# Kernel tuning notes

Hardware: AMD Instinct MI355X
Metric: run time of the kernel (lower is better)

## Reference

```python
import jax, jax.numpy as jnp
import numpy as np

SR = 22050
L = 65537            # signal length; chosen so rfft length == L (required by source broadcast)
NFFT = 131072        # 2**ceil(log2(L))
RLEN = NFFT // 2 + 1 # == L
OUT_SIZE = 65537     # output_size init arg
BANDS = [("delta", 1.0, 4.0), ("theta", 4.0, 8.0), ("alpha", 8.0, 13.0),
         ("beta", 13.0, 30.0), ("gamma", 30.0, 100.0), ("high_gamma", 100.0, 200.0)]
SPEC = [("schumann", 7.83), ("healing", 528.0), ("solfeggio", 396.0), ("sleep", 2.5),
        ("focus", 14.1), ("harmony", 432.0), ("meditation", 6.0), ("energy", 30.0)]
FREQS_NP = np.fft.rfftfreq(NFFT, d=1.0 / SR).astype(np.float32)


def _prog_mean(hp, W1, b1, W2, b2, W3, b3):
    # vectorized get_harmonic_progression(arange(L)).mean()
    t = jnp.arange(L, dtype=jnp.float32)
    tn = (t / OUT_SIZE)[:, None]                       # [L,1]
    h = jax.nn.relu(tn @ W1 + b1)
    h = jax.nn.relu(h @ W2 + b2)
    mp = h @ W3 + b3                                   # [L,8]
    mod_depth = mp[0, 1]
    chord_idx = jnp.floor(t * 8.0 / OUT_SIZE).astype(jnp.int32) % 8
    chord = hp[chord_idx]                              # [L,4]
    chord = chord * (1.0 + mod_depth * jnp.sin(2.0 * jnp.pi * t / OUT_SIZE))[:, None]
    return chord.mean()


def _gain(bw, fw, hp, W1, b1, W2, b2, W3, b3):
    # all modulation is data-independent -> single [RLEN] multiplicative gain
    t = jnp.arange(L, dtype=jnp.float32)
    gain = jnp.ones(RLEN, dtype=jnp.float32)
    for k, (_, low, high) in enumerate(BANDS):
        center = (low + high) / 2.0
        width = (high - low) / 2.0
        m_np = np.exp(-0.5 * ((FREQS_NP - center) / (width / 2.0)) ** 2)
        m_np[(FREQS_NP < low) | (FREQS_NP > high)] = 0.0
        if not np.any(m_np > 0.01):  # static branch (mask is data-independent)
            continue
        mask = jnp.asarray(m_np.astype(np.float32))     # [RLEN] == [L]
        time_mod = jnp.sin(2.0 * jnp.pi * center * t / SR)
        gain = gain * (1.0 + mask * bw[k] * (1.0 + 0.2 * time_mod))
    pm = _prog_mean(hp, W1, b1, W2, b2, W3, b3)
    ws = min(15, NFFT // 100)
    ws = ws if ws > 0 else 1
    for j, (_, f) in enumerate(SPEC):
        if f >= SR / 2:
            continue
        for mult in (1.0, 2.0, 3.0, 4.0, 5.0):
            hf = f * mult
            if hf >= SR / 2:
                continue
            hidx = int(np.argmin(np.abs(FREQS_NP - hf)))
            s = max(0, hidx - ws)
            e = min(RLEN - 1, hidx + ws)
            if s >= e:
                continue
            idxs = np.arange(s, e + 1)
            win = jnp.asarray(np.exp(-0.5 * ((idxs - hidx) / (ws / 3.0)) ** 2).astype(np.float32))
            enh = fw[j] * win * (1.0 / mult ** 1.2) * (1.0 + pm)
            gain = gain.at[s:e + 1].multiply(1.0 + enh)
    return gain


def _forward(x, bw, fw, hp, W1, b1, W2, b2, W3, b3):
    gain = _gain(bw, fw, hp, W1, b1, W2, b2, W3, b3)    # [RLEN]
    xp = jnp.pad(x, ((0, 0), (0, 0), (0, NFFT - L)))    # zero-pad to n_fft
    X = jnp.fft.rfft(xp, axis=-1) * gain                # [B,C,RLEN] complex
    mag = jnp.abs(X)
    ph = jnp.angle(X)
    mid = 0.7 * mag[..., 1:-1] + 0.15 * mag[..., :-2] + 0.15 * mag[..., 2:]
    mag_s = jnp.concatenate([mag[..., :1], mid, mag[..., -1:]], axis=-1)
    Xc = mag_s * jnp.exp(1j * ph)
    y = jnp.fft.irfft(Xc, n=NFFT, axis=-1)[..., :L]
    return y.astype(x.dtype)


def setup_inputs() -> dict:
    key = jax.random.key(0)
    ks = jax.random.split(key, 8)
    B, C = 128, 2
    x = jax.random.normal(ks[0], (B, C, L), dtype=jnp.float32)
    band_weights = jnp.full((6,), 0.5, dtype=jnp.float32)
    freq_weights = jnp.full((8,), 0.3, dtype=jnp.float32)
    harmonic_progression = jax.random.normal(ks[1], (8, 4), dtype=jnp.float32)
    W1 = jax.random.normal(ks[2], (1, 32), dtype=jnp.float32)
    b1 = jnp.zeros((32,), dtype=jnp.float32)
    W2 = jax.random.normal(ks[3], (32, 16), dtype=jnp.float32) * (1.0 / np.sqrt(32.0))
    b2 = jnp.zeros((16,), dtype=jnp.float32)
    W3 = jax.random.normal(ks[4], (16, 8), dtype=jnp.float32) * (1.0 / np.sqrt(16.0))
    b3 = jnp.zeros((8,), dtype=jnp.float32)
    return {"x": x, "band_weights": band_weights, "freq_weights": freq_weights,
            "harmonic_progression": harmonic_progression,
            "W1": W1, "b1": b1, "W2": W2, "b2": b2, "W3": W3, "b3": b3}


def reference(x, band_weights, freq_weights, harmonic_progression, W1, b1, W2, b2, W3, b3):
    return _forward(x, band_weights, freq_weights, harmonic_progression, W1, b1, W2, b2, W3, b3)
```

## Files before the change

### kernel.cpp

```cpp
#include <hip/hip_runtime.h>
#include <hip/hip_fp16.h>
#include <math.h>

#define L_SIG 65537
#define NH    65536
#define NSIG  256
#define PI_F  3.14159265358979323846f

struct alignas(8) c32 { float x, y; };
typedef __half2 h2;
__device__ __forceinline__ c32 mkc(float a, float b){ c32 r; r.x=a; r.y=b; return r; }
__device__ __forceinline__ c32 cadd(c32 a, c32 b){ return mkc(a.x+b.x, a.y+b.y); }
__device__ __forceinline__ c32 csub(c32 a, c32 b){ return mkc(a.x-b.x, a.y-b.y); }
__device__ __forceinline__ c32 cmul(c32 a, c32 b){ return mkc(a.x*b.x - a.y*b.y, a.x*b.y + a.y*b.x); }
__device__ __forceinline__ h2  c2h(c32 a){ return __floats2half2_rn(a.x, a.y); }
__device__ __forceinline__ c32 h2c(h2 a){ float2 f = __half22float2(a); return mkc(f.x, f.y); }

template<int S>
__device__ __forceinline__ void fft16(c32 v[16]) {
  constexpr float C16[16] = {
    1.0f, 0.9238795325112867f, 0.7071067811865476f, 0.3826834323650898f,
    0.0f,-0.3826834323650898f,-0.7071067811865476f,-0.9238795325112867f,
   -1.0f,-0.9238795325112867f,-0.7071067811865476f,-0.3826834323650898f,
    0.0f, 0.3826834323650898f, 0.7071067811865476f, 0.9238795325112867f };
  constexpr float S16[16] = {
    0.0f, 0.3826834323650898f, 0.7071067811865476f, 0.9238795325112867f,
    1.0f, 0.9238795325112867f, 0.7071067811865476f, 0.3826834323650898f,
    0.0f,-0.3826834323650898f,-0.7071067811865476f,-0.9238795325112867f,
   -1.0f,-0.9238795325112867f,-0.7071067811865476f,-0.3826834323650898f };
  c32 s[16];
  #pragma unroll
  for (int b0 = 0; b0 < 4; ++b0) {
    c32 x0=v[b0], x1=v[b0+4], x2=v[b0+8], x3=v[b0+12];
    c32 u0=cadd(x0,x2), u1=csub(x0,x2), u2=cadd(x1,x3), u3=csub(x1,x3);
    c32 iu3 = mkc(-u3.y, u3.x);
    c32 yy[4];
    yy[0]=cadd(u0,u2); yy[2]=csub(u0,u2);
    if (S < 0) { yy[1]=csub(u1,iu3); yy[3]=cadd(u1,iu3); }
    else       { yy[1]=cadd(u1,iu3); yy[3]=csub(u1,iu3); }
    #pragma unroll
    for (int c0 = 0; c0 < 4; ++c0) {
      const int p = (b0*c0) & 15;
      c32 w = mkc(C16[p], (S<0) ? -S16[p] : S16[p]);
      s[c0*4 + b0] = cmul(yy[c0], w);
    }
  }
  #pragma unroll
  for (int c0 = 0; c0 < 4; ++c0) {
    c32 x0=s[c0*4+0], x1=s[c0*4+1], x2=s[c0*4+2], x3=s[c0*4+3];
    c32 u0=cadd(x0,x2), u1=csub(x0,x2), u2=cadd(x1,x3), u3=csub(x1,x3);
    c32 iu3 = mkc(-u3.y, u3.x);
    c32 yy[4];
    yy[0]=cadd(u0,u2); yy[2]=csub(u0,u2);
    if (S < 0) { yy[1]=csub(u1,iu3); yy[3]=cadd(u1,iu3); }
    else       { yy[1]=cadd(u1,iu3); yy[3]=csub(u1,iu3); }
    v[c0+0]=yy[0]; v[c0+4]=yy[1]; v[c0+8]=yy[2]; v[c0+12]=yy[3];
  }
}

template<int S>
__device__ __forceinline__ void fft256_team(c32 v[16], int r, int t, c32* sc) {
  fft16<S>(v);
  float ang = (float)S * (2.0f*PI_F/256.0f) * (float)r;
  c32 st; __sincosf(ang, &st.y, &st.x);
  c32 w = st;
  #pragma unroll
  for (int c = 1; c < 16; ++c) { v[c] = cmul(v[c], w); w = cmul(w, st); }
  __syncthreads();
  #pragma unroll
  for (int c = 0; c < 16; ++c) {
    int idx = c*256 + ((r*16 + t) ^ ((c & 3) << 3));
    sc[idx] = v[c];
  }
  __syncthreads();
  #pragma unroll
  for (int a = 0; a < 16; ++a) {
    int idx = r*256 + ((a*16 + t) ^ ((r & 3) << 3));
    v[a] = sc[idx];
  }
  fft16<S>(v);
}

__global__ __launch_bounds__(256) void k_pm(const float* __restrict__ hp,
                                            float* __restrict__ pm_part) {
  __shared__ float r0[256], r1[256];
  int t = threadIdx.x, b = blockIdx.x;
  int gid = b*256 + t;
  float s0 = 0.f, s1 = 0.f;
  for (int tt = gid; tt < 65537; tt += 16384) {
    int ci = (tt * 8) / 65537;
    float cs = hp[ci*4+0] + hp[ci*4+1] + hp[ci*4+2] + hp[ci*4+3];
    float ang = (6.2831853071795864769f * (float)tt) / 65537.0f;
    s0 += cs;
    s1 += cs * sinf(ang);
  }
  r0[t] = s0; r1[t] = s1;
  __syncthreads();
  for (int s = 128; s > 0; s >>= 1) {
    if (t < s) { r0[t] += r0[t+s]; r1[t] += r1[t+s]; }
    __syncthreads();
  }
  if (t == 0) { pm_part[2*b] = r0[0]; pm_part[2*b+1] = r1[0]; }
}

__global__ __launch_bounds__(256) void k_prep2(const float* __restrict__ b1,
    const float* __restrict__ W2, const float* __restrict__ b2,
    const float* __restrict__ W3, const float* __restrict__ b3,
    const float* __restrict__ fw, const float* __restrict__ pm_part,
    float* __restrict__ pm_out, int* __restrict__ hidx, float* __restrict__ amp) {
  __shared__ float r0[64], r1[64];
  __shared__ float s_pm;
  int t = threadIdx.x;
  if (t < 64) { r0[t] = pm_part[2*t]; r1[t] = pm_part[2*t+1]; }
  __syncthreads();
  if (t == 0) {
    float h1[32], h2v[16];
    for (int i=0;i<32;i++){ float z = b1[i]; h1[i] = z > 0.f ? z : 0.f; }
    for (int o=0;o<16;o++){ float acc = b2[o];
      for (int i=0;i<32;i++) acc += h1[i]*W2[i*16+o];
      h2v[o] = acc > 0.f ? acc : 0.f; }
    float md = b3[1];
    for (int i=0;i<16;i++) md += h2v[i]*W3[i*8+1];
    float S0 = 0.f, S1 = 0.f;
    for (int i=0;i<64;i++){ S0 += r0[i]; S1 += r1[i]; }
    s_pm = (S0 + md*S1) / (65537.0f * 4.0f);
    pm_out[0] = s_pm;
  }
  __syncthreads();
  if (t < 40) {
    const double SPECF[8] = {7.83, 528.0, 396.0, 2.5, 14.1, 432.0, 6.0, 30.0};
    int j = t / 5, mi = t % 5;
    double mult = (double)(mi + 1);
    double hf = SPECF[j] * mult;
    double ratio = hf * (131072.0 / 22050.0);
    hidx[t] = (int)floor(ratio + 0.5);
    amp[t] = (float)((double)fw[j] * pow(mult, -1.2) * (1.0 + (double)s_pm));
  }
}

__global__ __launch_bounds__(256) void k_gain(float* __restrict__ gain,
    const float* __restrict__ bw, const int* __restrict__ hidx,
    const float* __restrict__ amp) {
  int i = blockIdx.x*256 + threadIdx.x;
  if (i >= 65537) return;
  float f = (float)((double)i * (22050.0/131072.0));
  float g = 1.0f;
  constexpr double LO[6] = {1,4,8,13,30,100};
  constexpr double HI[6] = {4,8,13,30,100,200};
  #pragma unroll
  for (int k = 0; k < 6; ++k) {
    float center = (float)(0.5*(LO[k]+HI[k]));
    float sig    = (float)(0.25*(HI[k]-LO[k]));
    float dm = (f - center)/sig;
    float mask = expf(-0.5f*dm*dm);
    if (f < (float)LO[k] || f > (float)HI[k]) mask = 0.f;
    float ang = (float)(6.283185307179586*0.5*(LO[k]+HI[k])) * (float)i / 22050.0f;
    g *= 1.0f + mask * bw[k] * (1.0f + 0.2f*sinf(ang));
  }
  for (int l = 0; l < 40; ++l) {
    int d = i - hidx[l];
    if (d >= -15 && d <= 15) {
      float dd = (float)d * 0.2f;
      g *= 1.0f + amp[l] * expf(-0.5f*dd*dd);
    }
  }
  gain[i] = g;
}

__global__ __launch_bounds__(256) void k_fwd1(const float* __restrict__ x,
                                              h2* __restrict__ A, int s0) {
  __shared__ c32 sc[4096];
  int b = blockIdx.x; int sl = b >> 4; int g = b & 15;
  int t = threadIdx.x & 15, r = threadIdx.x >> 4;
  int n1 = g*16 + t;
  const float* xb = x + (size_t)(s0 + sl) * L_SIG;
  c32 v[16];
  #pragma unroll
  for (int j = 0; j < 16; ++j) {
    int n = n1 + 256*r + 4096*j;
    c32 z = mkc(0.f, 0.f);
    if (n < 32768)       { z.x = xb[2*n]; z.y = xb[2*n+1]; }
    else if (n == 32768) { z.x = xb[65536]; }
    v[j] = z;
  }
  fft256_team<-1>(v, r, t, sc);
  float a0 = -(2.0f*PI_F/65536.0f) * (float)(n1 * r);
  float a1 = -(2.0f*PI_F/4096.0f)  * (float)n1;
  c32 wb, wst;
  __sincosf(a0, &wb.y, &wb.x);
  __sincosf(a1, &wst.y, &wst.x);
  #pragma unroll
  for (int j = 0; j < 16; ++j) { v[j] = cmul(v[j], wb); wb = cmul(wb, wst); }
  __syncthreads();
  #pragma unroll
  for (int j = 0; j < 16; ++j)
    sc[(r + 16*j)*16 + t] = v[j];
  __syncthreads();
  h2* Ab = A + (size_t)sl * NH;
  int u = threadIdx.x & 15, k2b = threadIdx.x >> 4;
  #pragma unroll
  for (int m = 0; m < 16; ++m) {
    int k2 = k2b + 16*m;
    Ab[(size_t)k2*256 + g*16 + u] = c2h(sc[k2*16 + u]);
  }
}

__global__ __launch_bounds__(256) void k_fwd2(const h2* __restrict__ A,
                                              h2* __restrict__ B) {
  __shared__ c32 sc[4096];
  h2* stg = (h2*)sc;
  int b = blockIdx.x; int sl = b >> 4; int g = b & 15;
  int tid = threadIdx.x;
  int t = tid & 15, r = tid >> 4;
  const h2* Ab = A + (size_t)sl * NH;
  #pragma unroll
  for (int m = 0; m < 4; ++m) {
    int flat = tid + 256*m;
    int row = flat >> 6, i = flat & 63;
    float4 z = ((const float4*)(Ab + (size_t)(g*16 + row)*256))[i];
    *((float4*)&stg[row*260 + 4*i]) = z;
  }
  __syncthreads();
  c32 v[16];
  #pragma unroll
  for (int j = 0; j < 16; ++j)
    v[j] = h2c(stg[t*260 + r + 16*j]);
  fft256_team<-1>(v, r, t, sc);
  h2* Bb = B + (size_t)sl * NH;
  int k2 = g*16 + t;
  #pragma unroll
  for (int j = 0; j < 16; ++j) Bb[(size_t)k2 + 256*(r + 16*j)] = c2h(v[j]);
}

__global__ __launch_bounds__(256) void k_mid(const h2* __restrict__ Z,
    h2* __restrict__ Zc, const float* __restrict__ gain) {
  __shared__ c32 XL[258], XH[258];
  __shared__ float ML[258], MH[258];
  __shared__ float TC[258], TS[258];
  int b = blockIdx.x; int s = b >> 7; int blk = b & 127;
  int k0 = blk << 8;
  const h2* Zs = Z + (size_t)s * NH;
  h2* Os = Zc + (size_t)s * NH;
  int t = threadIdx.x;
  for (int e = t; e < 258; e += 256) {
    int k = k0 - 1 + e;
    bool kv = (k >= 0);
    int kc = kv ? k : 0;
    c32 zk = h2c(Zs[k & (NH-1)]);
    c32 zb = h2c(Zs[(NH - k) & (NH-1)]);
    c32 Aa = mkc(0.5f*(zk.x + zb.x), 0.5f*(zk.y - zb.y));
    c32 Bm = mkc(0.5f*(zk.x - zb.x), 0.5f*(zk.y + zb.y));
    float sn, cn; __sincosf((PI_F/65536.0f)*(float)k, &sn, &cn);
    TC[e] = cn; TS[e] = sn;
    c32 wB = cmul(mkc(-sn, -cn), Bm);
    float gk = gain[kc];
    float gK = gain[NH - kc];
    c32 Xk = mkc((Aa.x + wB.x)*gk,  (Aa.y + wB.y)*gk);
    c32 XK = mkc((Aa.x - wB.x)*gK, -(Aa.y - wB.y)*gK);
    float nk = Xk.x*Xk.x + Xk.y*Xk.y;
    float nK = XK.x*XK.x + XK.y*XK.y;
    float rk = rsqrtf(nk), rK = rsqrtf(nK);
    c32 Uk = (nk > 0.f) ? mkc(Xk.x*rk, Xk.y*rk) : mkc(1.f, 0.f);
    c32 UK = (nK > 0.f) ? mkc(XK.x*rK, XK.y*rK) : mkc(1.f, 0.f);
    float mk = (kv && nk > 0.f) ? nk*rk : 0.f;
    float mK = (kv && nK > 0.f) ? nK*rK : 0.f;
    XL[e] = Uk;  ML[e] = mk;
    XH[257-e] = UK; MH[257-e] = mK;
  }
  __syncthreads();
  {
    int q = t; int k = k0 + q;
    float m = ML[q+1];
    float msm = (k == 0) ? m : 0.7f*m + 0.15f*(ML[q] + ML[q+2]);
    c32 U = XL[q+1];
    c32 XcL = mkc(U.x*msm, U.y*msm);
    int K = NH - k;
    int eH = 256 - q;
    float mh = MH[eH];
    float msh = (K == 65536) ? mh : 0.7f*mh + 0.15f*(MH[eH-1] + MH[eH+1]);
    c32 Uh = XH[eH];
    c32 XcH = mkc(Uh.x*msh, Uh.y*msh);
    c32 E = mkc(0.5f*(XcL.x + XcH.x), 0.5f*(XcL.y - XcH.y));
    c32 D = mkc(0.5f*(XcL.x - XcH.x), 0.5f*(XcL.y + XcH.y));
    c32 O = cmul(mkc(TC[q+1], TS[q+1]), D);
    const float invN = 1.0f/65536.0f;
    Os[k] = c2h(mkc((E.x - O.y)*invN, (E.y + O.x)*invN));
    if (k != 0) Os[K] = c2h(mkc((E.x + O.y)*invN, (O.x - E.y)*invN));
  }
  if (blk == 127 && t == 0) {
    float m = ML[257];
    float msm = 0.7f*m + 0.15f*(ML[256] + MH[1]);
    c32 U = XL[257];
    const float invN = 1.0f/65536.0f;
    Os[32768] = c2h(mkc(U.x*msm*invN, -U.y*msm*invN));
  }
}

__global__ __launch_bounds__(256) void k_inv1(const h2* __restrict__ Zc,
                                              h2* __restrict__ B) {
  __shared__ c32 sc[4096];
  int b = blockIdx.x; int sl = b >> 4; int g = b & 15;
  int t = threadIdx.x & 15, r = threadIdx.x >> 4;
  int a = g*16 + t;
  const h2* Zs = Zc + (size_t)sl * NH;
  c32 v[16];
  #pragma unroll
  for (int j = 0; j < 16; ++j) v[j] = h2c(Zs[(size_t)a + 256*(r + 16*j)]);
  fft256_team<1>(v, r, t, sc);
  float a0 = (2.0f*PI_F/65536.0f) * (float)(a * r);
  float a1 = (2.0f*PI_F/4096.0f)  * (float)a;
  c32 wb, wst;
  __sincosf(a0, &wb.y, &wb.x);
  __sincosf(a1, &wst.y, &wst.x);
  #pragma unroll
  for (int j = 0; j < 16; ++j) { v[j] = cmul(v[j], wb); wb = cmul(wb, wst); }
  __syncthreads();
  #pragma unroll
  for (int j = 0; j < 16; ++j)
    sc[(r + 16*j)*16 + t] = v[j];
  __syncthreads();
  h2* Bb = B + (size_t)sl * NH;
  int u = threadIdx.x & 15, m2b = threadIdx.x >> 4;
  #pragma unroll
  for (int m = 0; m < 16; ++m) {
    int m2 = m2b + 16*m;
    Bb[(size_t)m2*256 + g*16 + u] = c2h(sc[m2*16 + u]);
  }
}

__global__ __launch_bounds__(256) void k_inv2(const h2* __restrict__ B,
                                              float* __restrict__ out, int s0) {
  __shared__ c32 sc[4096];
  h2* stg = (h2*)sc;
  int b = blockIdx.x; int sl = b >> 4; int g = b & 15;
  int tid = threadIdx.x;
  int t = tid & 15, r = tid >> 4;
  const h2* Bb = B + (size_t)sl * NH;
  #pragma unroll
  for (int m = 0; m < 4; ++m) {
    int flat = tid + 256*m;
    int row = flat >> 6, i = flat & 63;
    float4 z = ((const float4*)(Bb + (size_t)(g*16 + row)*256))[i];
    *((float4*)&stg[row*260 + 4*i]) = z;
  }
  __syncthreads();
  c32 v[16];
  #pragma unroll
  for (int j = 0; j < 16; ++j)
    v[j] = h2c(stg[t*260 + r + 16*j]);
  fft256_team<1>(v, r, t, sc);
  float* yb = out + (size_t)(s0 + sl) * L_SIG;
  int m2 = g*16 + t;
  #pragma unroll
  for (int j = 0; j < 16; ++j) {
    int m1 = r + 16*j;
    if (m1 <= 127) {
      int m = m2 + 256*m1;
      yb[2*m]   = v[j].x;
      yb[2*m+1] = v[j].y;
    } else if (m1 == 128 && m2 == 0) {
      yb[65536] = v[j].x;
    }
  }
}

extern "C" void kernel_launch(void* const* d_in, const int* in_sizes, int n_in,
                              void* d_out, int out_size, void* d_ws, size_t ws_size,
                              hipStream_t stream) {
  const float* x  = (const float*)d_in[0];
  const float* bw = (const float*)d_in[1];
  const float* fw = (const float*)d_in[2];
  const float* hp = (const float*)d_in[3];
  const float* b1 = (const float*)d_in[5];
  const float* W2 = (const float*)d_in[6];
  const float* b2 = (const float*)d_in[7];
  const float* W3 = (const float*)d_in[8];
  const float* b3 = (const float*)d_in[9];
  float* out = (float*)d_out;
  char* ws = (char*)d_ws;

  const size_t perSig = (size_t)NH * sizeof(h2);
  const size_t tail   = (size_t)L_SIG * sizeof(float) + 2048;
  size_t cap = (ws_size > tail) ? (ws_size - tail) / (2*perSig) : 1;
  int chunk = (cap >= (size_t)NSIG) ? NSIG : (cap < 1 ? 1 : (int)cap);

  h2*    A    = (h2*)ws;
  h2*    Bb   = (h2*)(ws + (size_t)chunk*perSig);
  float* gain = (float*)(ws + 2*(size_t)chunk*perSig);
  float* pm   = gain + L_SIG;
  int*   hidx = (int*)(pm + 1);
  float* amp  = (float*)(hidx + 40);
  float* pm_part = amp + 40;

  k_pm   <<<64, 256, 0, stream>>>(hp, pm_part);
  k_prep2<<<1,  256, 0, stream>>>(b1, W2, b2, W3, b3, fw, pm_part, pm, hidx, amp);
  k_gain <<<257,256, 0, stream>>>(gain, bw, hidx, amp);

  for (int s0 = 0; s0 < NSIG; s0 += chunk) {
    int S = (NSIG - s0 < chunk) ? (NSIG - s0) : chunk;
    k_fwd1<<<S*16, 256, 0, stream>>>(x, A, s0);
    k_fwd2<<<S*16, 256, 0, stream>>>(A, Bb);
    k_mid <<<S*128,256, 0, stream>>>(Bb, A, gain);
    k_inv1<<<S*16, 256, 0, stream>>>(A, Bb);
    k_inv2<<<S*16, 256, 0, stream>>>(Bb, out, s0);
  }
}
```

Measured before the change: 277.8 us.

## Halve FFT shared memory via two-phase transpose and half-precision staging

The 256-point team transpose now runs in two phases, each handling half the threads, so the shared scratch shrinks from 4096 complex floats (32 KB) to 2048 complex values. The output staging now stores half2 values in shared memory instead of complex floats, and launch bounds request 8 blocks per CU to raise occupancy. k_inv1 also remaps its block indices to change the order in which column groups are scheduled. In exchange the transpose needs two extra barriers and leaves half the threads idle during each phase.

```diff
diff --git a/kernel.cpp b/kernel.cpp
--- a/kernel.cpp
+++ b/kernel.cpp
@@ -66,17 +66,31 @@
   c32 w = st;
   #pragma unroll
   for (int c = 1; c < 16; ++c) { v[c] = cmul(v[c], w); w = cmul(w, st); }
-  __syncthreads();
-  #pragma unroll
-  for (int c = 0; c < 16; ++c) {
-    int idx = c*256 + ((r*16 + t) ^ ((c & 3) << 3));
-    sc[idx] = v[c];
-  }
-  __syncthreads();
-  #pragma unroll
-  for (int a = 0; a < 16; ++a) {
-    int idx = r*256 + ((a*16 + t) ^ ((r & 3) << 3));
-    v[a] = sc[idx];
+  int p  = r*8 + (t & 7);
+  int fr = (r & 1) << 3;
+  __syncthreads();
+  if (t < 8) {
+    #pragma unroll
+    for (int c = 0; c < 16; ++c)
+      sc[c*128 + (p ^ ((c & 1) << 3))] = v[c];
+  }
+  __syncthreads();
+  if (t < 8) {
+    #pragma unroll
+    for (int a = 0; a < 16; ++a)
+      v[a] = sc[r*128 + ((a*8 + (t & 7)) ^ fr)];
+  }
+  __syncthreads();
+  if (t >= 8) {
+    #pragma unroll
+    for (int c = 0; c < 16; ++c)
+      sc[c*128 + (p ^ ((c & 1) << 3))] = v[c];
+  }
+  __syncthreads();
+  if (t >= 8) {
+    #pragma unroll
+    for (int a = 0; a < 16; ++a)
+      v[a] = sc[r*128 + ((a*8 + (t & 7)) ^ fr)];
   }
   fft16<S>(v);
 }
@@ -167,9 +181,11 @@
   gain[i] = g;
 }
 
-__global__ __launch_bounds__(256) void k_fwd1(const float* __restrict__ x,
-                                              h2* __restrict__ A, int s0) {
-  __shared__ c32 sc[4096];
+__global__ __launch_bounds__(256, 8) void k_fwd1(const float* __restrict__ x,
+                                                 h2* __restrict__ A, int s0) {
+  __shared__ float smem[4096];
+  c32* sc = (c32*)smem;
+  h2*  stg = (h2*)smem;
   int b = blockIdx.x; int sl = b >> 4; int g = b & 15;
   int t = threadIdx.x & 15, r = threadIdx.x >> 4;
   int n1 = g*16 + t;
@@ -194,21 +210,22 @@
   __syncthreads();
   #pragma unroll
   for (int j = 0; j < 16; ++j)
-    sc[(r + 16*j)*16 + t] = v[j];
+    stg[(r + 16*j)*16 + t] = c2h(v[j]);
   __syncthreads();
   h2* Ab = A + (size_t)sl * NH;
   int u = threadIdx.x & 15, k2b = threadIdx.x >> 4;
   #pragma unroll
   for (int m = 0; m < 16; ++m) {
     int k2 = k2b + 16*m;
-    Ab[(size_t)k2*256 + g*16 + u] = c2h(sc[k2*16 + u]);
-  }
-}
-
-__global__ __launch_bounds__(256) void k_fwd2(const h2* __restrict__ A,
-                                              h2* __restrict__ B) {
-  __shared__ c32 sc[4096];
-  h2* stg = (h2*)sc;
+    Ab[(size_t)k2*256 + g*16 + u] = stg[k2*16 + u];
+  }
+}
+
+__global__ __launch_bounds__(256, 8) void k_fwd2(const h2* __restrict__ A,
+                                                 h2* __restrict__ B) {
+  __shared__ float smem[4160];
+  c32* sc = (c32*)smem;
+  h2* stg = (h2*)smem;
   int b = blockIdx.x; int sl = b >> 4; int g = b & 15;
   int tid = threadIdx.x;
   int t = tid & 15, r = tid >> 4;
@@ -296,10 +313,15 @@
   }
 }
 
-__global__ __launch_bounds__(256) void k_inv1(const h2* __restrict__ Zc,
-                                              h2* __restrict__ B) {
-  __shared__ c32 sc[4096];
-  int b = blockIdx.x; int sl = b >> 4; int g = b & 15;
+__global__ __launch_bounds__(256, 8) void k_inv1(const h2* __restrict__ Zc,
+                                                 h2* __restrict__ B) {
+  __shared__ float smem[4096];
+  c32* sc = (c32*)smem;
+  h2*  stg = (h2*)smem;
+  int b = blockIdx.x;
+  int idx = b >> 3;
+  int sl = idx >> 1;
+  int g = ((b & 7) << 1) | (idx & 1);
   int t = threadIdx.x & 15, r = threadIdx.x >> 4;
   int a = g*16 + t;
   const h2* Zs = Zc + (size_t)sl * NH;
@@ -317,21 +339,22 @@
   __syncthreads();
   #pragma unroll
   for (int j = 0; j < 16; ++j)
-    sc[(r + 16*j)*16 + t] = v[j];
+    stg[(r + 16*j)*16 + t] = c2h(v[j]);
   __syncthreads();
   h2* Bb = B + (size_t)sl * NH;
   int u = threadIdx.x & 15, m2b = threadIdx.x >> 4;
   #pragma unroll
   for (int m = 0; m < 16; ++m) {
     int m2 = m2b + 16*m;
-    Bb[(size_t)m2*256 + g*16 + u] = c2h(sc[m2*16 + u]);
-  }
-}
-
-__global__ __launch_bounds__(256) void k_inv2(const h2* __restrict__ B,
-                                              float* __restrict__ out, int s0) {
-  __shared__ c32 sc[4096];
-  h2* stg = (h2*)sc;
+    Bb[(size_t)m2*256 + g*16 + u] = stg[m2*16 + u];
+  }
+}
+
+__global__ __launch_bounds__(256, 8) void k_inv2(const h2* __restrict__ B,
+                                                 float* __restrict__ out, int s0) {
+  __shared__ float smem[4160];
+  c32* sc = (c32*)smem;
+  h2* stg = (h2*)smem;
   int b = blockIdx.x; int sl = b >> 4; int g = b & 15;
   int tid = threadIdx.x;
   int t = tid & 15, r = tid >> 4;
```

Result: slower. 564.8 us (+103.3%).
